# Kernel tuning notes

Hardware: AMD Instinct MI355X
Metric: run time of the kernel (lower is better)

## Reference

```python
import jax, jax.numpy as jnp
import numpy as np

N_NODES = 50000
N_EDGES = 800000
D = 128


def gin_layer(x, edge_index, edge_attr, ee1, ee2, W1, b1, W2, b2):
    # PyG default flow source_to_target: x_j = x[edge_index[0]], aggregate at edge_index[1]
    src, dst = edge_index[0], edge_index[1]
    edge_emb = ee1[edge_attr[:, 0]] + ee2[edge_attr[:, 1]]           # [E, D]
    msg = x[src] + edge_emb                                          # [E, D]
    aggr = jax.ops.segment_sum(msg, dst, num_segments=x.shape[0])    # [N, D]
    h = jax.nn.relu(aggr @ W1 + b1)                                  # [N, 2D]
    return h @ W2 + b2                                               # [N, out]


def setup_inputs() -> dict:
    key = jax.random.key(0)
    ks = jax.random.split(key, 16)
    s = 1.0 / np.sqrt(D)
    inp = {
        "x": jax.random.normal(ks[0], (N_NODES, D), jnp.float32),
        "edge_index": jax.random.randint(ks[1], (2, N_EDGES), 0, N_NODES, dtype=jnp.int32),
        "edge_attr": jax.random.randint(ks[2], (N_EDGES, 2), 0, 3, dtype=jnp.int32),
        "ee1_0": jax.random.normal(ks[3], (6, D), jnp.float32) * s,
        "ee2_0": jax.random.normal(ks[4], (3, D), jnp.float32) * s,
        "W1_0": jax.random.normal(ks[5], (D, 2 * D), jnp.float32) * s,
        "b1_0": jnp.zeros((2 * D,), jnp.float32),
        "W2_0": jax.random.normal(ks[6], (2 * D, D), jnp.float32) * s,
        "b2_0": jnp.zeros((D,), jnp.float32),
        "ee1_1": jax.random.normal(ks[7], (6, D), jnp.float32) * s,
        "ee2_1": jax.random.normal(ks[8], (3, D), jnp.float32) * s,
        "W1_1": jax.random.normal(ks[9], (D, 2 * D), jnp.float32) * s,
        "b1_1": jnp.zeros((2 * D,), jnp.float32),
        "W2_1": jax.random.normal(ks[10], (2 * D, D), jnp.float32) * s,
        "b2_1": jnp.zeros((D,), jnp.float32),
    }
    return inp


def reference(x, edge_index, edge_attr, ee1_0, ee2_0, W1_0, b1_0, W2_0, b2_0,
              ee1_1, ee2_1, W1_1, b1_1, W2_1, b2_1):
    h = gin_layer(x, edge_index, edge_attr, ee1_0, ee2_0, W1_0, b1_0, W2_0, b2_0)
    h = jax.nn.relu(h)  # activation between GNN layers
    out = gin_layer(h, edge_index, edge_attr, ee1_1, ee2_1, W1_1, b1_1, W2_1, b2_1)
    return out  # jk='last'
```

## Files before the change

### kernel.cpp

```cpp
#include <hip/hip_runtime.h>

typedef __attribute__((ext_vector_type(8))) short s16x8;
typedef __attribute__((ext_vector_type(4))) float f32x4;
typedef unsigned short u16;
typedef unsigned char u8;
typedef unsigned long long u64;

#define D_FEAT 128
#define TILE1 4096

__device__ __forceinline__ u16 f2bf(float f) {
    unsigned u = __builtin_bit_cast(unsigned, f);
    u = u + 0x7fffu + ((u >> 16) & 1u);
    return (u16)(u >> 16);
}

__global__ __launch_bounds__(256) void prep_kernel(
        const float4* __restrict__ X4, u16* __restrict__ xb, int n4, int nbA,
        const int* __restrict__ dst, int* __restrict__ ghist, int E, int nb1, int bins,
        const float* __restrict__ ee1_0, const float* __restrict__ ee2_0,
        const float* __restrict__ ee1_1, const float* __restrict__ ee2_1,
        float* __restrict__ emb,
        const float* __restrict__ W1_0, const float* __restrict__ W2_0,
        const float* __restrict__ W1_1, const float* __restrict__ W2_1,
        u16* __restrict__ wout) {
    __shared__ int h[256];
    const int t = threadIdx.x;
    int b = blockIdx.x;

    if (b < nbA) {
        int i = b * 256 + t;
        if (i < n4) {
            float4 v = X4[i];
            uint2 p;
            p.x = (unsigned)f2bf(v.x) | ((unsigned)f2bf(v.y) << 16);
            p.y = (unsigned)f2bf(v.z) | ((unsigned)f2bf(v.w) << 16);
            *(uint2*)(xb + (size_t)i * 4) = p;
        }
        return;
    }
    b -= nbA;
    if (b < nb1) {
        h[t] = 0;
        __syncthreads();
        const int base = b * TILE1;
        #pragma unroll
        for (int j = 0; j < TILE1 / 256; ++j) {
            int e = base + j * 256 + t;
            if (e < E) atomicAdd(&h[dst[e] >> 8], 1);
        }
        __syncthreads();
        if (t < bins) ghist[t * nb1 + b] = h[t];
        return;
    }
    b -= nb1;
    if (b < 18) {
        int gi = b * 256 + t;
        int layer = gi / 2304;
        int rem = gi - layer * 2304;
        int code = rem >> 7;
        int d = rem & 127;
        int a0 = code / 3, a1 = code - a0 * 3;
        const float* e1 = layer ? ee1_1 : ee1_0;
        const float* e2 = layer ? ee2_1 : ee2_0;
        emb[layer * 2304 + code * 128 + d] = e1[a0 * 128 + d] + e2[a1 * 128 + d];
        return;
    }
    b -= 18;
    {
        int mat = b >> 7;
        const float* s = (mat == 0) ? W1_0 : (mat == 1) ? W2_0 : (mat == 2) ? W1_1 : W2_1;
        int K = (mat & 1) ? 256 : 128;
        int Nc = 384 - K;
        u16* d = wout + mat * 32768;
        int idx = (b & 127) * 256 + t;
        int n = idx / K, k = idx - n * K;
        d[idx] = f2bf(s[k * Nc + n]);
    }
}

__global__ __launch_bounds__(256) void scan1a_kernel(int* __restrict__ ghist,
                                                     int* __restrict__ btot, int nb1) {
    __shared__ int wt[4];
    const int t = threadIdx.x, lane = t & 63, wid = t >> 6;
    const int bin = blockIdx.x;
    const int v = (t < nb1) ? ghist[bin * nb1 + t] : 0;
    int s = v;
    #pragma unroll
    for (int off = 1; off < 64; off <<= 1) {
        int u = __shfl_up(s, off, 64);
        if (lane >= off) s += u;
    }
    if (lane == 63) wt[wid] = s;
    __syncthreads();
    int add = 0;
    #pragma unroll
    for (int w = 0; w < 4; ++w) add += (w < wid) ? wt[w] : 0;
    s += add;
    if (t < nb1) ghist[bin * nb1 + t] = s - v;
    if (t == 255) btot[bin] = s;
}

__global__ __launch_bounds__(256) void scatter1_kernel(const int* __restrict__ src,
                                                       const int* __restrict__ dst,
                                                       const int* __restrict__ eattr,
                                                       const int* __restrict__ ghist,
                                                       const int* __restrict__ btot,
                                                       u64* __restrict__ buf1,
                                                       int E, int nb1, int bins) {
    __shared__ int lofs[256];
    __shared__ int wt[4];
    const int t = threadIdx.x, lane = t & 63, wid = t >> 6;
    const int v = (t < bins) ? btot[t] : 0;
    int s = v;
    #pragma unroll
    for (int off = 1; off < 64; off <<= 1) {
        int u = __shfl_up(s, off, 64);
        if (lane >= off) s += u;
    }
    if (lane == 63) wt[wid] = s;
    __syncthreads();
    int add = 0;
    #pragma unroll
    for (int w = 0; w < 4; ++w) add += (w < wid) ? wt[w] : 0;
    s += add;
    if (t < bins) lofs[t] = (s - v) + ghist[t * nb1 + blockIdx.x];
    __syncthreads();

    const int base = blockIdx.x * TILE1;
    #pragma unroll
    for (int j = 0; j < TILE1 / 256; ++j) {
        int e = base + j * 256 + t;
        if (e < E) {
            int d = dst[e];
            int2 at = ((const int2*)eattr)[e];
            unsigned pay = (unsigned)src[e] | ((unsigned)(at.x * 3 + at.y) << 16);
            int pos = atomicAdd(&lofs[d >> 8], 1);
            buf1[pos] = ((u64)(unsigned)d << 32) | pay;
        }
    }
}

__global__ __launch_bounds__(1024) void bucket2_kernel(const u64* __restrict__ buf1,
                                                       const int* __restrict__ btot,
                                                       int* __restrict__ row_start,
                                                       unsigned* __restrict__ edges,
                                                       unsigned* __restrict__ countsw,
                                                       int N, int bins) {
    __shared__ int cnt[256];
    __shared__ int cur[256];
    __shared__ int wts[4];
    __shared__ unsigned ccnt[256 * 18];
    __shared__ int sb[2];
    const int t = threadIdx.x, lane = t & 63, wid = t >> 6;
    const int bin = blockIdx.x;

    int v0 = 0, s0 = 0;
    if (t < 256) {
        v0 = (t < bins) ? btot[t] : 0;
        s0 = v0;
        #pragma unroll
        for (int off = 1; off < 64; off <<= 1) {
            int u = __shfl_up(s0, off, 64);
            if (lane >= off) s0 += u;
        }
        if (lane == 63) wts[wid] = s0;
        cnt[t] = 0;
    }
    for (int i = t; i < 256 * 18; i += 1024) ccnt[i] = 0;
    __syncthreads();
    if (t < 256) {
        int add = 0;
        #pragma unroll
        for (int w = 0; w < 4; ++w) add += (w < wid) ? wts[w] : 0;
        s0 += add;
        if (t == bin) { sb[0] = s0 - v0; sb[1] = s0; }
    }
    __syncthreads();
    const int lo = sb[0], hi = sb[1];

    for (int i = lo + t; i < hi; i += 1024)
        atomicAdd(&cnt[(int)(buf1[i] >> 32) & 255], 1);
    __syncthreads();

    int v1 = 0, s1 = 0;
    if (t < 256) {
        v1 = cnt[t];
        s1 = v1;
        #pragma unroll
        for (int off = 1; off < 64; off <<= 1) {
            int u = __shfl_up(s1, off, 64);
            if (lane >= off) s1 += u;
        }
        if (lane == 63) wts[wid] = s1;
    }
    __syncthreads();
    if (t < 256) {
        int add = 0;
        #pragma unroll
        for (int w = 0; w < 4; ++w) add += (w < wid) ? wts[w] : 0;
        s1 += add;
        const int g = bin * 256 + t;
        if (g < N) row_start[g + 1] = lo + s1;
        cur[t] = s1 - v1;
        if (bin == 0 && t == 0) row_start[0] = 0;
    }
    __syncthreads();

    for (int i = lo + t; i < hi; i += 1024) {
        u64 rec = buf1[i];
        const int local = (int)(rec >> 32) & 255;
        int loc = atomicAdd(&cur[local], 1);
        edges[lo + loc] = (unsigned)rec;
        atomicAdd(&ccnt[local * 18 + ((unsigned)rec >> 16)], 1);
    }
    __syncthreads();

    if (t < 256) {
        const int g = bin * 256 + t;
        if (g < N) {
            unsigned w[5] = {0, 0, 0, 0, 0};
            #pragma unroll
            for (int c = 0; c < 18; ++c)
                w[c >> 2] |= ccnt[t * 18 + c] << (8 * (c & 3));
            #pragma unroll
            for (int k = 0; k < 5; ++k)
                countsw[(size_t)g * 5 + k] = w[k];
        }
    }
}

__global__ __launch_bounds__(256) void aggregate_kernel(const u16* __restrict__ X,
                                                        const int* __restrict__ row_start,
                                                        const unsigned* __restrict__ edges,
                                                        const float* __restrict__ emb,
                                                        const unsigned* __restrict__ countsw,
                                                        u16* __restrict__ A, int N) {
    __shared__ float semb[18 * 128];
    for (int i = threadIdx.x; i < 18 * 128; i += 256) semb[i] = emb[i];
    __syncthreads();
    const int node = blockIdx.x * 4 + (threadIdx.x >> 6);
    const int lane = threadIdx.x & 63;
    if (node >= N) return;

    unsigned cw[5];
    #pragma unroll
    for (int k = 0; k < 5; ++k) cw[k] = countsw[(size_t)node * 5 + k];

    int s = __builtin_amdgcn_readfirstlane(row_start[node]);
    const int e = __builtin_amdgcn_readfirstlane(row_start[node + 1]);
    const float2* sem2 = (const float2*)semb;
    float a0 = 0.f, a1 = 0.f;

    while (s < e) {
        const int take = (e - s < 64) ? (e - s) : 64;
        unsigned pl = edges[s + (lane < take ? lane : 0)];
        #pragma unroll
        for (int c = 0; c < 4; ++c) {
            const int cb = c * 16;
            if (cb < take) {
                unsigned ps[16];
                unsigned xv[16];
                #pragma unroll
                for (int j = 0; j < 16; ++j)
                    ps[j] = __builtin_amdgcn_readlane(pl, cb + j);
                #pragma unroll
                for (int j = 0; j < 16; ++j)
                    xv[j] = *(const unsigned*)(X + (ps[j] & 0xFFFFu) * D_FEAT + lane * 2);
                #pragma unroll
                for (int j = 0; j < 16; ++j) {
                    const float m = (cb + j < take) ? 1.f : 0.f;
                    a0 += m * __builtin_bit_cast(float, xv[j] << 16);
                    a1 += m * __builtin_bit_cast(float, xv[j] & 0xFFFF0000u);
                }
            }
        }
        s += take;
    }

    #pragma unroll
    for (int w = 0; w < 5; ++w) {
        #pragma unroll
        for (int b = 0; b < 4; ++b) {
            const int code = w * 4 + b;
            if (code < 18) {
                const float cf = (float)((cw[w] >> (8 * b)) & 255u);
                float2 ev = sem2[code * 64 + lane];
                a0 += cf * ev.x;
                a1 += cf * ev.y;
            }
        }
    }

    unsigned outp = (unsigned)f2bf(a0) | ((unsigned)f2bf(a1) << 16);
    *(unsigned*)(A + node * D_FEAT + lane * 2) = outp;
}

template <bool RELU2, bool OUTF32>
__global__ __launch_bounds__(256, 1) void mlp_kernel(const u16* __restrict__ A,
                                                     const u16* __restrict__ B1t,
                                                     const float* __restrict__ bias1,
                                                     const u16* __restrict__ B2t,
                                                     const float* __restrict__ bias2,
                                                     void* __restrict__ C, int M, int nt) {
    extern __shared__ __align__(16) u16 lds[];
    u16* w1 = lds;
    u16* w2 = lds + 32768;
    u16* hh = lds + 65536;
    const int tid = threadIdx.x;
    const int wave = tid >> 6;
    const int lane = tid & 63;
    const int m16 = lane & 15;
    const int quad = lane >> 4;

    {
        const uint4* src1 = (const uint4*)B1t;
        const uint4* src2 = (const uint4*)B2t;
        #pragma unroll
        for (int i = 0; i < 16; ++i) {
            int s = i * 256 + tid;
            uint4 v = src1[s];
            int c = (((s >> 8) * 4 + ((s >> 2) & 3)) << 6) | ((s & 3) << 4) | ((s >> 4) & 15);
            *(uint4*)(w1 + c * 8) = v;
        }
        #pragma unroll
        for (int i = 0; i < 16; ++i) {
            int s = i * 256 + tid;
            uint4 v = src2[s];
            int c = (((s >> 9) * 8 + ((s >> 2) & 7)) << 6) | ((s & 3) << 4) | ((s >> 5) & 15);
            *(uint4*)(w2 + c * 8) = v;
        }
    }
    float b1v[16];
    #pragma unroll
    for (int t = 0; t < 16; ++t) b1v[t] = bias1[t * 16 + m16];
    float b2v[8];
    #pragma unroll
    for (int t = 0; t < 8; ++t) b2v[t] = bias2[t * 16 + m16];

    const int hbase = wave * 4096;

    int tile = blockIdx.x;
    s16x8 af[4];
    #pragma unroll
    for (int kb = 0; kb < 4; ++kb) af[kb] = s16x8{};
    if (tile < nt) {
        const int arow = tile * 64 + wave * 16 + m16;
        if (arow < M) {
            #pragma unroll
            for (int kb = 0; kb < 4; ++kb)
                af[kb] = *(const s16x8*)(A + (size_t)arow * 128 + kb * 32 + quad * 8);
        }
    }

    __syncthreads();

    for (; tile < nt; tile += 256) {
        const int row0 = tile * 64 + wave * 16;

        f32x4 acc[16];
        #pragma unroll
        for (int t = 0; t < 16; ++t) acc[t] = f32x4{0, 0, 0, 0};
        #pragma unroll
        for (int kb = 0; kb < 4; ++kb) {
            #pragma unroll
            for (int t = 0; t < 16; ++t) {
                s16x8 bf = *(const s16x8*)(w1 + (((((t << 2) | kb) << 6) | lane) * 8));
                acc[t] = __builtin_amdgcn_mfma_f32_16x16x32_bf16(af[kb], bf, acc[t], 0, 0, 0);
            }
        }

        const int ntile = tile + 256;
        s16x8 afn[4];
        #pragma unroll
        for (int kb = 0; kb < 4; ++kb) afn[kb] = s16x8{};
        if (ntile < nt) {
            const int arow = ntile * 64 + wave * 16 + m16;
            if (arow < M) {
                #pragma unroll
                for (int kb = 0; kb < 4; ++kb)
                    afn[kb] = *(const s16x8*)(A + (size_t)arow * 128 + kb * 32 + quad * 8);
            }
        }

        #pragma unroll
        for (int t = 0; t < 16; ++t) {
            const int col = t * 16 + m16;
            #pragma unroll
            for (int r = 0; r < 4; ++r) {
                const int row = quad * 4 + r;
                float v = acc[t][r] + b1v[t];
                v = v > 0.f ? v : 0.f;
                hh[(hbase + row * 256 + col) ^ ((row & 7) << 3)] = f2bf(v);
            }
        }
        __syncthreads();

        f32x4 acc2[8];
        #pragma unroll
        for (int t = 0; t < 8; ++t) acc2[t] = f32x4{0, 0, 0, 0};
        #pragma unroll
        for (int kb = 0; kb < 8; ++kb) {
            s16x8 haf = *(const s16x8*)(hh + ((hbase + m16 * 256 + kb * 32 + quad * 8) ^ ((m16 & 7) << 3)));
            #pragma unroll
            for (int t = 0; t < 8; ++t) {
                s16x8 bf = *(const s16x8*)(w2 + (((((t << 3) | kb) << 6) | lane) * 8));
                acc2[t] = __builtin_amdgcn_mfma_f32_16x16x32_bf16(haf, bf, acc2[t], 0, 0, 0);
            }
        }

        #pragma unroll
        for (int t = 0; t < 8; ++t) {
            const int col = t * 16 + m16;
            #pragma unroll
            for (int r = 0; r < 4; ++r) {
                const int row = row0 + quad * 4 + r;
                if (row < M) {
                    float v = acc2[t][r] + b2v[t];
                    if (RELU2) v = v > 0.f ? v : 0.f;
                    if (OUTF32) ((float*)C)[(size_t)row * 128 + col] = v;
                    else        ((u16*)C)[(size_t)row * 128 + col] = f2bf(v);
                }
            }
        }
        __syncthreads();

        #pragma unroll
        for (int kb = 0; kb < 4; ++kb) af[kb] = afn[kb];
    }
}

extern "C" void kernel_launch(void* const* d_in, const int* in_sizes, int n_in,
                              void* d_out, int out_size, void* d_ws, size_t ws_size,
                              hipStream_t stream) {
    const int N = in_sizes[0] / D_FEAT;
    const int E = in_sizes[1] / 2;

    const float* x    = (const float*)d_in[0];
    const int* eidx   = (const int*)d_in[1];
    const int* eattr  = (const int*)d_in[2];
    const float* ee1_0 = (const float*)d_in[3];
    const float* ee2_0 = (const float*)d_in[4];
    const float* W1_0  = (const float*)d_in[5];
    const float* b1_0  = (const float*)d_in[6];
    const float* W2_0  = (const float*)d_in[7];
    const float* b2_0  = (const float*)d_in[8];
    const float* ee1_1 = (const float*)d_in[9];
    const float* ee2_1 = (const float*)d_in[10];
    const float* W1_1  = (const float*)d_in[11];
    const float* b1_1  = (const float*)d_in[12];
    const float* W2_1  = (const float*)d_in[13];
    const float* b2_1  = (const float*)d_in[14];

    const int nb1  = (E + TILE1 - 1) / TILE1;
    const int bins = (N + 255) / 256;

    char* ws = (char*)d_ws;
    size_t off = 0;
    auto alloc = [&](size_t bytes) { size_t o = off; off = (off + bytes + 255) & ~(size_t)255; return o; };
    size_t o_rowstart = alloc((size_t)(N + 1) * 4);
    size_t o_edges    = alloc((size_t)E * 4);
    size_t o_ghist    = alloc((size_t)bins * nb1 * 4);
    size_t o_btot     = alloc((size_t)bins * 4);
    size_t o_counts   = alloc((size_t)N * 20);
    size_t o_emb      = alloc(2 * 18 * 128 * 4);
    size_t o_wt       = alloc(4 * 32768 * 2);
    size_t o_aa       = alloc((size_t)N * D_FEAT * 2);

    int*      row_start = (int*)(ws + o_rowstart);
    unsigned* edges     = (unsigned*)(ws + o_edges);
    int*      ghist     = (int*)(ws + o_ghist);
    int*      btot      = (int*)(ws + o_btot);
    unsigned* countsw   = (unsigned*)(ws + o_counts);
    float*    emb       = (float*)(ws + o_emb);
    u16*      W1t_0     = (u16*)(ws + o_wt);
    u16*      W2t_0     = W1t_0 + 32768;
    u16*      W1t_1     = W2t_0 + 32768;
    u16*      W2t_1     = W1t_1 + 32768;
    u16*      AA        = (u16*)(ws + o_aa);
    u64*      buf1      = (u64*)(ws + o_aa);

    u16* X2 = (u16*)d_out;
    u16* xb = (u16*)d_out + (size_t)N * D_FEAT;

    const int nt = (N + 63) / 64;
    const int aggB = (N + 3) / 4;
    const int n4 = N * D_FEAT / 4;
    const int nbA = (n4 + 255) / 256;
    const int LDS_MLP = 163840;

    static bool attr_done = false;
    if (!attr_done) {
        hipFuncSetAttribute((const void*)mlp_kernel<true, false>,
                            hipFuncAttributeMaxDynamicSharedMemorySize, LDS_MLP);
        hipFuncSetAttribute((const void*)mlp_kernel<false, true>,
                            hipFuncAttributeMaxDynamicSharedMemorySize, LDS_MLP);
        attr_done = true;
    }

    prep_kernel<<<nbA + nb1 + 18 + 512, 256, 0, stream>>>(
        (const float4*)x, xb, n4, nbA,
        eidx + E, ghist, E, nb1, bins,
        ee1_0, ee2_0, ee1_1, ee2_1, emb,
        W1_0, W2_0, W1_1, W2_1, W1t_0);

    scan1a_kernel<<<bins, 256, 0, stream>>>(ghist, btot, nb1);
    scatter1_kernel<<<nb1, 256, 0, stream>>>(eidx, eidx + E, eattr, ghist, btot, buf1, E, nb1, bins);
    bucket2_kernel<<<bins, 1024, 0, stream>>>(buf1, btot, row_start, edges, countsw, N, bins);

    aggregate_kernel<<<aggB, 256, 0, stream>>>(xb, row_start, edges, emb, countsw, AA, N);
    mlp_kernel<true, false><<<256, 256, LDS_MLP, stream>>>(AA, W1t_0, b1_0, W2t_0, b2_0, X2, N, nt);

    aggregate_kernel<<<aggB, 256, 0, stream>>>(X2, row_start, edges, emb + 18 * 128, countsw, AA, N);
    mlp_kernel<false, true><<<256, 256, LDS_MLP, stream>>>(AA, W1t_1, b1_1, W2t_1, b2_1, d_out, N, nt);
}
```

Baseline: 264.1 us.

## Gather four edge rows per wave with 16-byte loads and cross-quad reduce

The aggregation kernel now splits each wave into four 16-lane groups, and each group handles a different edge. Every lane loads 8 bf16 features as a uint4 instead of one 32-bit pair per lane per edge. Partial sums are combined with xor shuffles across the quads, and lanes 0-15 write 16-byte outputs. This cuts the number of gather instructions per edge and widens the memory transactions. In exchange it adds shuffle reductions, uses more accumulator registers, and leaves lanes idle on the final store. The row_start allocation is also padded slightly.

```diff
diff --git a/kernel.cpp b/kernel.cpp
--- a/kernel.cpp
+++ b/kernel.cpp
@@ -242,6 +242,10 @@
     const int node = blockIdx.x * 4 + (threadIdx.x >> 6);
     const int lane = threadIdx.x & 63;
     if (node >= N) return;
+    const int quad = lane >> 4;
+    const int m16 = lane & 15;
+    const bool b16 = (lane & 16) != 0;
+    const bool b32 = (lane & 32) != 0;
 
     unsigned cw[5];
     #pragma unroll
@@ -249,51 +253,71 @@
 
     int s = __builtin_amdgcn_readfirstlane(row_start[node]);
     const int e = __builtin_amdgcn_readfirstlane(row_start[node + 1]);
-    const float2* sem2 = (const float2*)semb;
-    float a0 = 0.f, a1 = 0.f;
+
+    float acc[8];
+    #pragma unroll
+    for (int k = 0; k < 8; ++k) acc[k] = 0.f;
 
     while (s < e) {
         const int take = (e - s < 64) ? (e - s) : 64;
         unsigned pl = edges[s + (lane < take ? lane : 0)];
         #pragma unroll
-        for (int c = 0; c < 4; ++c) {
-            const int cb = c * 16;
-            if (cb < take) {
-                unsigned ps[16];
-                unsigned xv[16];
-                #pragma unroll
-                for (int j = 0; j < 16; ++j)
-                    ps[j] = __builtin_amdgcn_readlane(pl, cb + j);
-                #pragma unroll
-                for (int j = 0; j < 16; ++j)
-                    xv[j] = *(const unsigned*)(X + (ps[j] & 0xFFFFu) * D_FEAT + lane * 2);
-                #pragma unroll
-                for (int j = 0; j < 16; ++j) {
-                    const float m = (cb + j < take) ? 1.f : 0.f;
-                    a0 += m * __builtin_bit_cast(float, xv[j] << 16);
-                    a1 += m * __builtin_bit_cast(float, xv[j] & 0xFFFF0000u);
-                }
+        for (int g = 0; g < 16; ++g) {
+            if (g * 4 < take) {
+                const unsigned w0 = __builtin_amdgcn_readlane(pl, g * 4 + 0) & 0xFFFFu;
+                const unsigned w1 = __builtin_amdgcn_readlane(pl, g * 4 + 1) & 0xFFFFu;
+                const unsigned w2 = __builtin_amdgcn_readlane(pl, g * 4 + 2) & 0xFFFFu;
+                const unsigned w3 = __builtin_amdgcn_readlane(pl, g * 4 + 3) & 0xFFFFu;
+                const unsigned r01 = b16 ? w1 : w0;
+                const unsigned r23 = b16 ? w3 : w2;
+                const unsigned row = b32 ? r23 : r01;
+                const uint4 xv = *(const uint4*)(X + row * D_FEAT + m16 * 8);
+                const float mv = (g * 4 + quad < take) ? 1.f : 0.f;
+                acc[0] += mv * __builtin_bit_cast(float, xv.x << 16);
+                acc[1] += mv * __builtin_bit_cast(float, xv.x & 0xFFFF0000u);
+                acc[2] += mv * __builtin_bit_cast(float, xv.y << 16);
+                acc[3] += mv * __builtin_bit_cast(float, xv.y & 0xFFFF0000u);
+                acc[4] += mv * __builtin_bit_cast(float, xv.z << 16);
+                acc[5] += mv * __builtin_bit_cast(float, xv.z & 0xFFFF0000u);
+                acc[6] += mv * __builtin_bit_cast(float, xv.w << 16);
+                acc[7] += mv * __builtin_bit_cast(float, xv.w & 0xFFFF0000u);
             }
         }
         s += take;
     }
 
     #pragma unroll
-    for (int w = 0; w < 5; ++w) {
-        #pragma unroll
-        for (int b = 0; b < 4; ++b) {
-            const int code = w * 4 + b;
-            if (code < 18) {
-                const float cf = (float)((cw[w] >> (8 * b)) & 255u);
-                float2 ev = sem2[code * 64 + lane];
-                a0 += cf * ev.x;
-                a1 += cf * ev.y;
-            }
-        }
-    }
-
-    unsigned outp = (unsigned)f2bf(a0) | ((unsigned)f2bf(a1) << 16);
-    *(unsigned*)(A + node * D_FEAT + lane * 2) = outp;
+    for (int i = 0; i < 5; ++i) {
+        const int code = 4 * i + quad;
+        const bool valid = code < 18;
+        const int codeC = valid ? code : 0;
+        const float cf = valid ? (float)((cw[i] >> (8 * quad)) & 255u) : 0.f;
+        const float* ep = semb + codeC * 128 + m16 * 8;
+        const float4 e0 = *(const float4*)(ep);
+        const float4 e1 = *(const float4*)(ep + 4);
+        acc[0] += cf * e0.x;
+        acc[1] += cf * e0.y;
+        acc[2] += cf * e0.z;
+        acc[3] += cf * e0.w;
+        acc[4] += cf * e1.x;
+        acc[5] += cf * e1.y;
+        acc[6] += cf * e1.z;
+        acc[7] += cf * e1.w;
+    }
+
+    #pragma unroll
+    for (int k = 0; k < 8; ++k) acc[k] += __shfl_xor(acc[k], 16, 64);
+    #pragma unroll
+    for (int k = 0; k < 8; ++k) acc[k] += __shfl_xor(acc[k], 32, 64);
+
+    if (lane < 16) {
+        uint4 o;
+        o.x = (unsigned)f2bf(acc[0]) | ((unsigned)f2bf(acc[1]) << 16);
+        o.y = (unsigned)f2bf(acc[2]) | ((unsigned)f2bf(acc[3]) << 16);
+        o.z = (unsigned)f2bf(acc[4]) | ((unsigned)f2bf(acc[5]) << 16);
+        o.w = (unsigned)f2bf(acc[6]) | ((unsigned)f2bf(acc[7]) << 16);
+        *(uint4*)(A + (size_t)node * D_FEAT + lane * 8) = o;
+    }
 }
 
 template <bool RELU2, bool OUTF32>
@@ -458,7 +482,7 @@
     char* ws = (char*)d_ws;
     size_t off = 0;
     auto alloc = [&](size_t bytes) { size_t o = off; off = (off + bytes + 255) & ~(size_t)255; return o; };
-    size_t o_rowstart = alloc((size_t)(N + 1) * 4);
+    size_t o_rowstart = alloc((size_t)(N + 4) * 4);
     size_t o_edges    = alloc((size_t)E * 4);
     size_t o_ghist    = alloc((size_t)bins * nb1 * 4);
     size_t o_btot     = alloc((size_t)bins * 4);
```

Result: slower. 275.4 us (+4.3%).
